# Optimization experiments

Measured on AMD Instinct MI355X. Metric: run time of the kernel, lower is better.

The kernel has to match this reference:

```python
import jax, jax.numpy as jnp
import numpy as np

B, N, DIN, DOUT, H = 32, 1024, 512, 512, 8
DH = DOUT // H  # attn_dim = 64


def setup_inputs() -> dict:
    key = jax.random.key(0)
    k1, k2, k3, k4, k5 = jax.random.split(key, 5)
    X = jax.random.normal(k1, (B, N, DIN), dtype=jnp.float32)
    # adjacency mask (sparse-ish 0/1 pattern, self-loops included)
    A = (jax.random.uniform(k2, (B, N, N)) < 0.05).astype(jnp.float32)
    A = jnp.maximum(A, jnp.eye(N, dtype=jnp.float32)[None])
    # per-head projection weights/biases and bilinear coefficient matrices
    # (xavier_normal init as in param_initializer)
    std_w = np.sqrt(2.0 / (DIN + DH))
    std_c = np.sqrt(2.0 / (DH + DH))
    Wp = jax.random.normal(k3, (H, DIN, DH), dtype=jnp.float32) * std_w
    bp = jnp.zeros((H, DH), dtype=jnp.float32)
    C = jax.random.normal(k4, (H, DH, DH), dtype=jnp.float32) * std_c
    return {"X": X, "A": A, "Wp": Wp, "bp": bp, "C": C}


def reference(X, A, Wp, bp, C):
    # per-head linear projection: [B,H,N,DH]
    Xp = jnp.einsum('bnd,hdk->bhnk', X, Wp) + bp[None, :, None, :]
    # bilinear transform: torch.einsum('akj,ij->aki') == Xp @ C.T per head
    Xc = jnp.einsum('bhnk,hjk->bhnj', Xp, C)
    # attention scores [B,H,N,N], masked by adjacency, tanh
    # (dropout is identity in eval mode)
    attn = jnp.tanh(A[:, None] * jnp.einsum('bhnj,bhmj->bhnm', Xc, Xp))
    # aggregate: [B,H,N,DH]
    Xh = jnp.einsum('bhnm,bhmk->bhnk', attn, Xp)
    # concat heads along feature dim (head order matches torch.cat), then relu
    out = jnp.moveaxis(Xh, 1, 2).reshape(X.shape[0], X.shape[1], -1)
    return jax.nn.relu(out)
```

## Files before the change

kernel.cpp:

```cpp
#include <hip/hip_runtime.h>
#include <hip/hip_bf16.h>

typedef __attribute__((ext_vector_type(8))) _Float16 half8;
typedef __attribute__((ext_vector_type(4))) _Float16 half4;
typedef __attribute__((ext_vector_type(2))) unsigned uint2v;
typedef __attribute__((ext_vector_type(4))) float f32x4;

#define B_ 32
#define N_ 1024
#define DIN_ 512
#define H_ 8
#define DH_ 64

__device__ __forceinline__ float tanh_e(float x) {
    float e = __builtin_amdgcn_exp2f(x * 2.885390081777927f);
    float r = __builtin_amdgcn_rcpf(e + 1.f);
    return fmaf(-2.f, r, 1.f);
}

__device__ __forceinline__ half4 pack4(float a, float b, float c, float d) {
    auto lo = __builtin_amdgcn_cvt_pkrtz(a, b);
    auto hi = __builtin_amdgcn_cvt_pkrtz(c, d);
    uint2v u = { __builtin_bit_cast(unsigned, lo), __builtin_bit_cast(unsigned, hi) };
    return __builtin_bit_cast(half4, u);
}

__global__ __launch_bounds__(256) void pack_mask(const float* __restrict__ A,
                                                 unsigned long long* __restrict__ Abits) {
    int tid = blockIdx.x * 256 + threadIdx.x;
    int wave = tid >> 6;
    int lane = threadIdx.x & 63;
    float a = A[(size_t)wave * 64 + lane];
    unsigned long long m = __ballot(a != 0.f);
    if (lane == 0) Abits[wave] = m;
}

__global__ __launch_bounds__(256) void prep_w(const float* __restrict__ Wp,
                                              const float* __restrict__ C,
                                              _Float16* __restrict__ WT,
                                              _Float16* __restrict__ Cb) {
    int gid = blockIdx.x * 256 + threadIdx.x;
    if (gid < H_ * DH_ * DIN_) {
        int h = gid >> 15;
        int n = (gid >> 9) & 63;
        int k = gid & 511;
        WT[gid] = (_Float16)Wp[((size_t)(h * DIN_ + k)) * DH_ + n];
    } else {
        int cid = gid - H_ * DH_ * DIN_;
        if (cid < H_ * DH_ * DH_) Cb[cid] = (_Float16)C[cid];
    }
}

__global__ __launch_bounds__(256) void proj_gemm(const float* __restrict__ X,
                                                 const float* __restrict__ bp,
                                                 const _Float16* __restrict__ WT,
                                                 _Float16* __restrict__ Xp) {
    __shared__ _Float16 Xb[64][72];

    int tid = threadIdx.x;
    int lane = tid & 63, w = tid >> 6;
    int blk = blockIdx.x;
    int b = blk >> 5;
    int n0 = ((blk >> 1) & 15) * 64;
    int h = (blk & 1) * 4 + w;

    int r = tid >> 2, q = tid & 3;
    const float* xrow = X + ((size_t)b * N_ + n0 + r) * DIN_ + q * 16;

    f32x4 acc[4][4] = {};

    for (int kc = 0; kc < 8; ++kc) {
        float4 v0 = *(const float4*)(xrow + kc * 64 + 0);
        float4 v1 = *(const float4*)(xrow + kc * 64 + 4);
        float4 v2 = *(const float4*)(xrow + kc * 64 + 8);
        float4 v3 = *(const float4*)(xrow + kc * 64 + 12);
        half8 h0 = {(_Float16)v0.x, (_Float16)v0.y, (_Float16)v0.z, (_Float16)v0.w,
                    (_Float16)v1.x, (_Float16)v1.y, (_Float16)v1.z, (_Float16)v1.w};
        half8 h1 = {(_Float16)v2.x, (_Float16)v2.y, (_Float16)v2.z, (_Float16)v2.w,
                    (_Float16)v3.x, (_Float16)v3.y, (_Float16)v3.z, (_Float16)v3.w};
        *(half8*)&Xb[r][q * 16] = h0;
        *(half8*)&Xb[r][q * 16 + 8] = h1;
        __syncthreads();

#pragma unroll
        for (int ks = 0; ks < 2; ++ks) {
            half8 a[4];
#pragma unroll
            for (int m = 0; m < 4; ++m)
                a[m] = *(const half8*)&Xb[m * 16 + (lane & 15)][ks * 32 + (lane >> 4) * 8];
#pragma unroll
            for (int f = 0; f < 4; ++f) {
                half8 bb = *(const half8*)(WT + ((size_t)(h * 64 + f * 16 + (lane & 15))) * DIN_
                                           + kc * 64 + ks * 32 + (lane >> 4) * 8);
#pragma unroll
                for (int m = 0; m < 4; ++m)
                    acc[m][f] = __builtin_amdgcn_mfma_f32_16x16x32_f16(a[m], bb, acc[m][f], 0, 0, 0);
            }
        }
        __syncthreads();
    }

    size_t bh = (size_t)(b * 8 + h);
#pragma unroll
    for (int f = 0; f < 4; ++f) {
        int col = f * 16 + (lane & 15);
        float bias = bp[h * 64 + col];
#pragma unroll
        for (int m = 0; m < 4; ++m) {
            int row = m * 16 + ((lane >> 4) << 2);
#pragma unroll
            for (int j = 0; j < 4; ++j) {
                Xp[(bh * N_ + n0 + row + j) * DH_ + col] = (_Float16)(acc[m][f][j] + bias);
            }
        }
    }
}

__global__ __launch_bounds__(256) void bil_kernel(const _Float16* __restrict__ Xp,
                                                  const _Float16* __restrict__ Cb,
                                                  _Float16* __restrict__ Xc,
                                                  _Float16* __restrict__ XpT) {
    __shared__ _Float16 Xs[64][72];

    int tid = threadIdx.x;
    int lane = tid & 63, w = tid >> 6;
    int blk = blockIdx.x;
    int bh = blk >> 4;
    int n0 = (blk & 15) * 64;
    int h = bh & 7;

    int r = tid >> 2, q = tid & 3;
    const half8* src = (const half8*)(Xp + ((size_t)bh * N_ + n0 + r) * DH_ + q * 16);
    *(half8*)&Xs[r][q * 16] = src[0];
    *(half8*)&Xs[r][q * 16 + 8] = src[1];
    __syncthreads();

    f32x4 acc[4] = {{0,0,0,0},{0,0,0,0},{0,0,0,0},{0,0,0,0}};
#pragma unroll
    for (int ks = 0; ks < 2; ++ks) {
        half8 a = *(const half8*)&Xs[w * 16 + (lane & 15)][ks * 32 + (lane >> 4) * 8];
#pragma unroll
        for (int f = 0; f < 4; ++f) {
            half8 bb = *(const half8*)(Cb + ((size_t)(h * DH_ + f * 16 + (lane & 15))) * DH_
                                       + ks * 32 + (lane >> 4) * 8);
            acc[f] = __builtin_amdgcn_mfma_f32_16x16x32_f16(a, bb, acc[f], 0, 0, 0);
        }
    }
    int rb = w * 16 + ((lane >> 4) << 2);
#pragma unroll
    for (int f = 0; f < 4; ++f) {
        int col = f * 16 + (lane & 15);
#pragma unroll
        for (int j = 0; j < 4; ++j)
            Xc[((size_t)bh * N_ + n0 + rb + j) * DH_ + col] = (_Float16)acc[f][j];
    }

    {
        int d = (lane & 3) * 16 + (lane >> 2);
        __align__(16) _Float16 tmp[16];
#pragma unroll
        for (int i = 0; i < 16; ++i) tmp[i] = Xs[w * 16 + i][d];
        _Float16* dst = XpT + ((size_t)bh * DH_ + d) * N_ + n0 + w * 16;
        *(half8*)dst = *(half8*)tmp;
        *(half8*)(dst + 8) = *(half8*)(tmp + 8);
    }
}

__global__ __launch_bounds__(256) void attn_kernel(const _Float16* __restrict__ Xp,
                                                   const _Float16* __restrict__ Xc,
                                                   const _Float16* __restrict__ XpT,
                                                   const unsigned long long* __restrict__ Abits,
                                                   float* __restrict__ out) {
    __shared__ _Float16 Kb[64][72];
    __shared__ _Float16 Vt[64][72];

    int tid = threadIdx.x;
    int lane = tid & 63, w = tid >> 6;
    int hi = lane >> 4;
    int c16 = lane & 15;
    int blk = blockIdx.x;
    int bh = blk >> 4;
    int q0 = (blk & 15) * 64;
    int b = bh >> 3, h = bh & 7;

    const _Float16* qbase = Xc + ((size_t)bh * N_ + q0 + w * 16 + c16) * DH_ + hi * 8;
    half8 qa0 = *(const half8*)qbase;
    half8 qa1 = *(const half8*)(qbase + 32);

    int r = tid >> 2, q = tid & 3;
    const unsigned long long* mbase = Abits + ((size_t)b * N_ + q0 + w * 16 + c16) * 16;

    f32x4 oacc[4] = {{0,0,0,0},{0,0,0,0},{0,0,0,0},{0,0,0,0}};

    for (int mt = 0; mt < 16; ++mt) {
        __syncthreads();
        const half8* ksrc = (const half8*)(Xp + ((size_t)bh * N_ + mt * 64 + r) * DH_ + q * 16);
        half8 k0 = ksrc[0], k1 = ksrc[1];
        const half8* vsrc = (const half8*)(XpT + ((size_t)bh * DH_ + r) * N_ + mt * 64 + q * 16);
        half8 v0 = vsrc[0], v1 = vsrc[1];
        *(half8*)&Kb[r][q * 16] = k0;
        *(half8*)&Kb[r][q * 16 + 8] = k1;
        *(half8*)&Vt[r][q * 16] = v0;
        *(half8*)&Vt[r][q * 16 + 8] = v1;
        __syncthreads();

        f32x4 s[4] = {{0,0,0,0},{0,0,0,0},{0,0,0,0},{0,0,0,0}};
#pragma unroll
        for (int f = 0; f < 4; ++f) {
            half8 kb0 = *(const half8*)&Kb[f * 16 + c16][hi * 8];
            half8 kb1 = *(const half8*)&Kb[f * 16 + c16][32 + hi * 8];
            s[f] = __builtin_amdgcn_mfma_f32_16x16x32_f16(kb0, qa0, s[f], 0, 0, 0);
            s[f] = __builtin_amdgcn_mfma_f32_16x16x32_f16(kb1, qa1, s[f], 0, 0, 0);
        }

        unsigned long long m64 = mbase[mt] >> (hi * 4);
        unsigned mlo = (unsigned)m64;
        unsigned mhi32 = (unsigned)(m64 >> 32);

        half4 pa[4];
#pragma unroll
        for (int f = 0; f < 4; ++f) {
            unsigned dw = (f & 2) ? mhi32 : mlo;
            int bb = (f & 1) * 16;
            float t0 = tanh_e(s[f][0]) * (float)((dw >> bb) & 1u);
            float t1 = tanh_e(s[f][1]) * (float)((dw >> (bb + 1)) & 1u);
            float t2 = tanh_e(s[f][2]) * (float)((dw >> (bb + 2)) & 1u);
            float t3 = tanh_e(s[f][3]) * (float)((dw >> (bb + 3)) & 1u);
            pa[f] = pack4(t0, t1, t2, t3);
        }

#pragma unroll
        for (int f = 0; f < 4; ++f) {
            half4 vf0 = *(const half4*)&Vt[c16     ][f * 16 + hi * 4];
            half4 vf1 = *(const half4*)&Vt[16 + c16][f * 16 + hi * 4];
            half4 vf2 = *(const half4*)&Vt[32 + c16][f * 16 + hi * 4];
            half4 vf3 = *(const half4*)&Vt[48 + c16][f * 16 + hi * 4];
            oacc[0] = __builtin_amdgcn_mfma_f32_16x16x16f16(pa[f], vf0, oacc[0], 0, 0, 0);
            oacc[1] = __builtin_amdgcn_mfma_f32_16x16x16f16(pa[f], vf1, oacc[1], 0, 0, 0);
            oacc[2] = __builtin_amdgcn_mfma_f32_16x16x16f16(pa[f], vf2, oacc[2], 0, 0, 0);
            oacc[3] = __builtin_amdgcn_mfma_f32_16x16x16f16(pa[f], vf3, oacc[3], 0, 0, 0);
        }
    }

    int rb = w * 16 + hi * 4;
#pragma unroll
    for (int fo = 0; fo < 4; ++fo) {
        int col = h * DH_ + fo * 16 + c16;
#pragma unroll
        for (int j = 0; j < 4; ++j) {
            out[((size_t)b * N_ + q0 + rb + j) * 512 + col] = fmaxf(oacc[fo][j], 0.f);
        }
    }
}

extern "C" void kernel_launch(void* const* d_in, const int* in_sizes, int n_in,
                              void* d_out, int out_size, void* d_ws, size_t ws_size,
                              hipStream_t stream) {
    const float* X  = (const float*)d_in[0];
    const float* A  = (const float*)d_in[1];
    const float* Wp = (const float*)d_in[2];
    const float* bp = (const float*)d_in[3];
    const float* C  = (const float*)d_in[4];
    float* out = (float*)d_out;

    char* ws = (char*)d_ws;
    unsigned long long* Abits = (unsigned long long*)ws;
    _Float16* WT  = (_Float16*)(ws + 4u * 1024 * 1024);
    _Float16* Cb  = (_Float16*)(ws + 4u * 1024 * 1024 + 512 * 1024);
    _Float16* Xp  = (_Float16*)(ws + 5u * 1024 * 1024);
    _Float16* Xc  = (_Float16*)(ws + 37u * 1024 * 1024);
    _Float16* XpT = (_Float16*)(ws + 69u * 1024 * 1024);

    pack_mask<<<(B_ * N_ * N_) / (64 * 4), 256, 0, stream>>>(A, Abits);
    prep_w<<<(H_ * DH_ * DIN_ + H_ * DH_ * DH_ + 255) / 256, 256, 0, stream>>>(Wp, C, WT, Cb);
    proj_gemm<<<B_ * 16 * 2, 256, 0, stream>>>(X, bp, WT, Xp);
    bil_kernel<<<B_ * H_ * 16, 256, 0, stream>>>(Xp, Cb, Xc, XpT);
    attn_kernel<<<B_ * H_ * 16, 256, 0, stream>>>(Xp, Xc, XpT, Abits, out);
}
```

Baseline: 477.1 us.

## Prefetch next K/V tile in attention, coalesce XpT writes, fragment-order weights

The attention loop now loads the next tile's K, V and mask word into registers while the current tile is computed, hiding global-load latency behind MFMA work. The bilinear kernel stages the transposed Xp tile in shared memory so XpT is written with coalesced 16-byte rows. The weight prep kernel stores W in MFMA-fragment order so proj_gemm reads contiguous per-lane vectors. The changes cost extra registers and one more shared buffer and barrier.

```diff
diff --git a/kernel.cpp b/kernel.cpp
--- a/kernel.cpp
+++ b/kernel.cpp
@@ -37,14 +37,18 @@
 
 __global__ __launch_bounds__(256) void prep_w(const float* __restrict__ Wp,
                                               const float* __restrict__ C,
-                                              _Float16* __restrict__ WT,
+                                              _Float16* __restrict__ WTf,
                                               _Float16* __restrict__ Cb) {
     int gid = blockIdx.x * 256 + threadIdx.x;
     if (gid < H_ * DH_ * DIN_) {
-        int h = gid >> 15;
-        int n = (gid >> 9) & 63;
-        int k = gid & 511;
-        WT[gid] = (_Float16)Wp[((size_t)(h * DIN_ + k)) * DH_ + n];
+        int blk = gid >> 9;
+        int inner = gid & 511;
+        int f = blk & 3, ks = (blk >> 2) & 1, kc = (blk >> 3) & 7, h = blk >> 6;
+        int l = inner >> 3, j = inner & 7;
+        int c16 = l & 15, hi = l >> 4;
+        int n = f * 16 + c16;
+        int k = kc * 64 + ks * 32 + hi * 8 + j;
+        WTf[gid] = (_Float16)Wp[((size_t)(h * DIN_ + k)) * DH_ + n];
     } else {
         int cid = gid - H_ * DH_ * DIN_;
         if (cid < H_ * DH_ * DH_) Cb[cid] = (_Float16)C[cid];
@@ -53,7 +57,7 @@
 
 __global__ __launch_bounds__(256) void proj_gemm(const float* __restrict__ X,
                                                  const float* __restrict__ bp,
-                                                 const _Float16* __restrict__ WT,
+                                                 const _Float16* __restrict__ WTf,
                                                  _Float16* __restrict__ Xp) {
     __shared__ _Float16 Xb[64][72];
 
@@ -66,6 +70,7 @@
 
     int r = tid >> 2, q = tid & 3;
     const float* xrow = X + ((size_t)b * N_ + n0 + r) * DIN_ + q * 16;
+    const _Float16* wbase = WTf + (size_t)h * 32768 + lane * 8;
 
     f32x4 acc[4][4] = {};
 
@@ -90,8 +95,7 @@
                 a[m] = *(const half8*)&Xb[m * 16 + (lane & 15)][ks * 32 + (lane >> 4) * 8];
 #pragma unroll
             for (int f = 0; f < 4; ++f) {
-                half8 bb = *(const half8*)(WT + ((size_t)(h * 64 + f * 16 + (lane & 15))) * DIN_
-                                           + kc * 64 + ks * 32 + (lane >> 4) * 8);
+                half8 bb = *(const half8*)(wbase + (((kc * 2 + ks) * 4 + f) << 9));
 #pragma unroll
                 for (int m = 0; m < 4; ++m)
                     acc[m][f] = __builtin_amdgcn_mfma_f32_16x16x32_f16(a[m], bb, acc[m][f], 0, 0, 0);
@@ -121,6 +125,7 @@
                                                   _Float16* __restrict__ Xc,
                                                   _Float16* __restrict__ XpT) {
     __shared__ _Float16 Xs[64][72];
+    __shared__ _Float16 XsT[64][72];
 
     int tid = threadIdx.x;
     int lane = tid & 63, w = tid >> 6;
@@ -160,9 +165,16 @@
         __align__(16) _Float16 tmp[16];
 #pragma unroll
         for (int i = 0; i < 16; ++i) tmp[i] = Xs[w * 16 + i][d];
-        _Float16* dst = XpT + ((size_t)bh * DH_ + d) * N_ + n0 + w * 16;
-        *(half8*)dst = *(half8*)tmp;
-        *(half8*)(dst + 8) = *(half8*)(tmp + 8);
+        *(half8*)&XsT[d][w * 16] = *(half8*)tmp;
+        *(half8*)&XsT[d][w * 16 + 8] = *(half8*)(tmp + 8);
+    }
+    __syncthreads();
+
+    {
+        int d = tid >> 3;
+        int c8 = (tid & 7) * 8;
+        *(half8*)(XpT + ((size_t)bh * DH_ + d) * N_ + n0 + c8) = *(const half8*)&XsT[d][c8];
+        *(half8*)(XpT + ((size_t)bh * DH_ + d + 32) * N_ + n0 + c8) = *(const half8*)&XsT[d + 32][c8];
     }
 }
 
@@ -192,16 +204,26 @@
 
     f32x4 oacc[4] = {{0,0,0,0},{0,0,0,0},{0,0,0,0},{0,0,0,0}};
 
+    const _Float16* kptr = Xp + ((size_t)bh * N_ + r) * DH_ + q * 16;
+    const _Float16* vptr = XpT + ((size_t)bh * DH_ + r) * N_ + q * 16;
+    half8 k0 = *(const half8*)kptr, k1 = *(const half8*)(kptr + 8);
+    half8 v0 = *(const half8*)vptr, v1 = *(const half8*)(vptr + 8);
+    unsigned long long mcur = mbase[0];
+    unsigned long long mnext = 0;
+
     for (int mt = 0; mt < 16; ++mt) {
         __syncthreads();
-        const half8* ksrc = (const half8*)(Xp + ((size_t)bh * N_ + mt * 64 + r) * DH_ + q * 16);
-        half8 k0 = ksrc[0], k1 = ksrc[1];
-        const half8* vsrc = (const half8*)(XpT + ((size_t)bh * DH_ + r) * N_ + mt * 64 + q * 16);
-        half8 v0 = vsrc[0], v1 = vsrc[1];
         *(half8*)&Kb[r][q * 16] = k0;
         *(half8*)&Kb[r][q * 16 + 8] = k1;
         *(half8*)&Vt[r][q * 16] = v0;
         *(half8*)&Vt[r][q * 16 + 8] = v1;
+        if (mt < 15) {
+            const _Float16* kn = kptr + (size_t)(mt + 1) * 64 * DH_;
+            const _Float16* vn = vptr + (mt + 1) * 64;
+            k0 = *(const half8*)kn; k1 = *(const half8*)(kn + 8);
+            v0 = *(const half8*)vn; v1 = *(const half8*)(vn + 8);
+            mnext = mbase[mt + 1];
+        }
         __syncthreads();
 
         f32x4 s[4] = {{0,0,0,0},{0,0,0,0},{0,0,0,0},{0,0,0,0}};
@@ -213,7 +235,7 @@
             s[f] = __builtin_amdgcn_mfma_f32_16x16x32_f16(kb1, qa1, s[f], 0, 0, 0);
         }
 
-        unsigned long long m64 = mbase[mt] >> (hi * 4);
+        unsigned long long m64 = mcur >> (hi * 4);
         unsigned mlo = (unsigned)m64;
         unsigned mhi32 = (unsigned)(m64 >> 32);
 
@@ -240,6 +262,7 @@
             oacc[2] = __builtin_amdgcn_mfma_f32_16x16x16f16(pa[f], vf2, oacc[2], 0, 0, 0);
             oacc[3] = __builtin_amdgcn_mfma_f32_16x16x16f16(pa[f], vf3, oacc[3], 0, 0, 0);
         }
+        mcur = mnext;
     }
 
     int rb = w * 16 + hi * 4;
@@ -265,15 +288,15 @@
 
     char* ws = (char*)d_ws;
     unsigned long long* Abits = (unsigned long long*)ws;
-    _Float16* WT  = (_Float16*)(ws + 4u * 1024 * 1024);
+    _Float16* WTf = (_Float16*)(ws + 4u * 1024 * 1024);
     _Float16* Cb  = (_Float16*)(ws + 4u * 1024 * 1024 + 512 * 1024);
     _Float16* Xp  = (_Float16*)(ws + 5u * 1024 * 1024);
     _Float16* Xc  = (_Float16*)(ws + 37u * 1024 * 1024);
     _Float16* XpT = (_Float16*)(ws + 69u * 1024 * 1024);
 
     pack_mask<<<(B_ * N_ * N_) / (64 * 4), 256, 0, stream>>>(A, Abits);
-    prep_w<<<(H_ * DH_ * DIN_ + H_ * DH_ * DH_ + 255) / 256, 256, 0, stream>>>(Wp, C, WT, Cb);
-    proj_gemm<<<B_ * 16 * 2, 256, 0, stream>>>(X, bp, WT, Xp);
+    prep_w<<<(H_ * DH_ * DIN_ + H_ * DH_ * DH_ + 255) / 256, 256, 0, stream>>>(Wp, C, WTf, Cb);
+    proj_gemm<<<B_ * 16 * 2, 256, 0, stream>>>(X, bp, WTf, Xp);
     bil_kernel<<<B_ * H_ * 16, 256, 0, stream>>>(Xp, Cb, Xc, XpT);
     attn_kernel<<<B_ * H_ * 16, 256, 0, stream>>>(Xp, Xc, XpT, Abits, out);
 }
```

New measurement: 462.8 us. -3.0%, faster.
